# Performance work log

Measured on AMD Instinct MI355X. Metric: run time of the kernel, lower is better.

Reference implementation:

```python
import jax, jax.numpy as jnp
import numpy as np

NUM_CLASSES = 80
STRIDES = (8, 16, 32)


def bce_logits(x, t):
    # numerically stable BCEWithLogits, reduction='none'
    return jnp.maximum(x, 0.) - x * t + jnp.log1p(jnp.exp(-jnp.abs(x)))


def decode_level(feat, stride):
    # feat: [B, C, H, W] -> decoded [B, HW, C], grid x/y [HW], strides [HW]
    B, C, H, W = feat.shape
    out = feat.reshape(B, C, H * W).transpose(0, 2, 1)  # [B, HW, C]
    yv, xv = jnp.meshgrid(jnp.arange(H), jnp.arange(W), indexing='ij')
    grid = jnp.stack([xv, yv], axis=-1).reshape(-1, 2).astype(feat.dtype)  # [HW, 2]
    xy = (out[..., :2] + grid[None]) * stride
    wh = jnp.exp(out[..., 2:4]) * stride
    out = jnp.concatenate([xy, wh, out[..., 4:]], axis=-1)
    return out, grid[:, 0], grid[:, 1], jnp.full((H * W,), float(stride), feat.dtype)


def pairwise_iou_cxcywh(g, p):
    # g: [G,4] gt boxes, p: [A,4] pred boxes (cx,cy,w,h) -> [G,A]
    tl = jnp.maximum(g[:, None, :2] - g[:, None, 2:] * 0.5, p[None, :, :2] - p[None, :, 2:] * 0.5)
    br = jnp.minimum(g[:, None, :2] + g[:, None, 2:] * 0.5, p[None, :, :2] + p[None, :, 2:] * 0.5)
    area_g = g[:, 2] * g[:, 3]
    area_p = p[:, 2] * p[:, 3]
    en = jnp.all(tl < br, axis=-1)
    inter = jnp.prod(br - tl, axis=-1) * en
    return inter / (area_g[:, None] + area_p[None, :] - inter + 1e-16)


def simota_assign(gt_boxes, gt_cls, bbox_p, cls_p, obj_p, xc, yc, strides):
    # per-image SimOTA label assignment (masked, jit-friendly)
    # gt_boxes [G,4], gt_cls [G] int, bbox_p [A,4], cls_p [A,C], obj_p [A,1]
    G = gt_boxes.shape[0]
    A = bbox_p.shape[0]
    gl = gt_boxes[:, 0:1] - 0.5 * gt_boxes[:, 2:3]
    gr = gt_boxes[:, 0:1] + 0.5 * gt_boxes[:, 2:3]
    gt_ = gt_boxes[:, 1:2] - 0.5 * gt_boxes[:, 3:4]
    gb = gt_boxes[:, 1:2] + 0.5 * gt_boxes[:, 3:4]
    in_box = (xc[None] > gl) & (xc[None] < gr) & (yc[None] > gt_) & (yc[None] < gb)  # [G,A]
    r = 2.5 * strides[None]
    in_ctr = ((xc[None] > gt_boxes[:, 0:1] - r) & (xc[None] < gt_boxes[:, 0:1] + r)
              & (yc[None] > gt_boxes[:, 1:2] - r) & (yc[None] < gt_boxes[:, 1:2] + r))
    geom = in_box | in_ctr
    anchor_ok = jnp.any(geom, axis=0)        # fg_mask candidate anchors [A]
    in_both = in_box & in_ctr                # [G,A]

    ious = pairwise_iou_cxcywh(gt_boxes, bbox_p)            # [G,A]
    ious = jnp.where(anchor_ok[None], ious, 0.)
    iou_cost = -jnp.log(ious + 1e-8)

    eps = 1e-8
    p = jnp.sqrt(jax.nn.sigmoid(cls_p) * jax.nn.sigmoid(obj_p))  # [A,C]
    logp = jnp.log(p + eps)
    log1mp = jnp.log(1. - p + eps)
    base = -jnp.sum(log1mp, axis=-1)                              # [A]
    sel = (logp - log1mp)[:, gt_cls]                              # [A,G]
    cls_cost = base[None, :] - sel.T                              # [G,A] = BCE(p, onehot).sum(-1)

    cost = cls_cost + 3.0 * iou_cost + 100000.0 * (~in_both) + 1e9 * (~anchor_ok[None])

    n_cand = min(10, A)
    topk_ious = jax.lax.top_k(ious, n_cand)[0]                    # [G,10]
    dyn_k = jnp.maximum(jnp.sum(topk_ious, axis=1).astype(jnp.int32), 1)  # [G]
    rank = jnp.argsort(jnp.argsort(cost, axis=1), axis=1)         # rank of each anchor per gt
    matching = (rank < dyn_k[:, None]) & anchor_ok[None]          # [G,A] bool

    am = jnp.sum(matching, axis=0)                                # anchors matched to >1 gt
    argmin_g = jnp.argmin(cost, axis=0)                           # [A]
    best = jnp.arange(G)[:, None] == argmin_g[None]               # [G,A]
    matching = jnp.where(am[None] > 1, best, matching)

    fg = jnp.any(matching, axis=0)                                # [A]
    matched_gt = jnp.argmax(matching, axis=0)                     # [A]
    pred_iou = jnp.sum(matching * ious, axis=0)                   # [A]
    cls_t = jax.nn.one_hot(gt_cls[matched_gt], NUM_CLASSES, dtype=bbox_p.dtype) * pred_iou[:, None]
    reg_t = gt_boxes[matched_gt]                                  # [A,4]
    return fg, cls_t, reg_t


def iou_elem(p, t):
    # elementwise IoU between matched pred/target boxes (cxcywh), IOUloss 'iou'
    tl = jnp.maximum(p[..., :2] - p[..., 2:] * 0.5, t[..., :2] - t[..., 2:] * 0.5)
    br = jnp.minimum(p[..., :2] + p[..., 2:] * 0.5, t[..., :2] + t[..., 2:] * 0.5)
    ap = p[..., 2] * p[..., 3]
    ag = t[..., 2] * t[..., 3]
    en = jnp.all(tl < br, axis=-1).astype(p.dtype)
    ai = jnp.prod(br - tl, axis=-1) * en
    return ai / (ap + ag - ai + 1e-16)


def yolo_loss(feat8, feat16, feat32, labels):
    outs, xs, ys, ss = [], [], [], []
    for feat, s in zip((feat8, feat16, feat32), STRIDES):
        o, x, y, st = decode_level(feat, s)
        outs.append(o); xs.append(x); ys.append(y); ss.append(st)
    outputs = jnp.concatenate(outs, axis=1)            # [B, A, 5+C]
    x_shifts = jnp.concatenate(xs)
    y_shifts = jnp.concatenate(ys)
    strides = jnp.concatenate(ss)
    xc = (x_shifts + 0.5) * strides                    # anchor centers [A]
    yc = (y_shifts + 0.5) * strides

    bbox_preds = outputs[..., :4]
    obj_preds = outputs[..., 4]
    cls_preds = outputs[..., 5:5 + NUM_CLASSES]

    labels_sg = jax.lax.stop_gradient(labels)
    gt_boxes = labels_sg[..., :4]
    gt_cls = labels_sg[..., 4].astype(jnp.int32)

    # assignment is @torch.no_grad in the original -> stop_gradient on its inputs
    fg, cls_t, reg_t = jax.vmap(simota_assign, in_axes=(0, 0, 0, 0, 0, None, None, None))(
        gt_boxes, gt_cls,
        jax.lax.stop_gradient(bbox_preds),
        jax.lax.stop_gradient(cls_preds),
        jax.lax.stop_gradient(outputs[..., 4:5]),
        xc, yc, strides)

    fg_f = fg.astype(outputs.dtype)                    # [B, A]
    iou = iou_elem(bbox_preds, reg_t)                  # [B, A]
    loss_iou = jnp.sum(fg_f * (1. - iou ** 2))
    loss_obj = jnp.sum(bce_logits(obj_preds, fg_f))
    loss_cls = jnp.sum(fg_f[..., None] * bce_logits(cls_preds, cls_t))
    num_fg = jnp.maximum(jnp.sum(fg_f), 1.)
    loss = (5.0 * loss_iou + 0.1 * loss_obj + loss_cls) / num_fg
    return loss


def setup_inputs() -> dict:
    key = jax.random.key(0)
    k1, k2, k3, k4, k5, k6, k7 = jax.random.split(key, 7)
    B, G = 32, 30
    feat8 = jax.random.normal(k1, (B, 85, 80, 80), jnp.float32)
    feat16 = jax.random.normal(k2, (B, 85, 40, 40), jnp.float32)
    feat32 = jax.random.normal(k3, (B, 85, 20, 20), jnp.float32)
    cx = jax.random.uniform(k4, (B, G, 1), jnp.float32, 60., 580.)
    cy = jax.random.uniform(k5, (B, G, 1), jnp.float32, 60., 580.)
    wh = jax.random.uniform(k6, (B, G, 2), jnp.float32, 20., 150.)
    cls = jax.random.randint(k7, (B, G, 1), 0, NUM_CLASSES).astype(jnp.float32)
    labels = jnp.concatenate([cx, cy, wh, cls], axis=-1)   # [B, G, 5] = cx,cy,w,h,cls
    return {"feat8": feat8, "feat16": feat16, "feat32": feat32, "labels": labels}


def reference(feat8, feat16, feat32, labels):
    return yolo_loss(feat8, feat16, feat32, labels)
```

## Files before the change

kernel.cpp:

```cpp
#include <hip/hip_runtime.h>
#include <cstdint>
#include <cstddef>

#define NB 32
#define NG 30
#define NA 8400
#define NC 80
#define SELB 512
#define MGRIDX 33
#define NBLK (MGRIDX * NB)
#define LCAP 128
#define NITER 17

typedef unsigned long long u64;

struct Params {
  const float* f8; const float* f16; const float* f32; const float* lab;
  float*    bbox;
  float*    objlog;
  float*    po;
  float*    base_;
  uint2*    gob;
  unsigned* mmask;
  float*    part;
  float*    out;
};

__device__ __forceinline__ float fsigm(float x) {
  return __fdividef(1.0f, 1.0f + __expf(-x));
}

__device__ __forceinline__ void anchor_geom(int a, int& x, int& y, int& W, int& hw,
                                            float& stride, int& lvl) {
  if (a < 6400)      { W = 80; hw = 6400; stride = 8.f;  lvl = 0; int i = a;        y = i / 80; x = i - y * 80; }
  else if (a < 8000) { W = 40; hw = 1600; stride = 16.f; lvl = 1; int i = a - 6400; y = i / 40; x = i - y * 40; }
  else               { W = 20; hw = 400;  stride = 32.f; lvl = 2; int i = a - 8000; y = i / 20; x = i - y * 20; }
}

__device__ __forceinline__ float pair_iou(float px, float py, float pw, float ph,
                                          float glx, float gty, float grx, float gby,
                                          float area_g) {
  float tlx = fmaxf(glx, px - pw * 0.5f);
  float tly = fmaxf(gty, py - ph * 0.5f);
  float brx = fminf(grx, px + pw * 0.5f);
  float bry = fminf(gby, py + ph * 0.5f);
  float inter = ((tlx < brx) && (tly < bry)) ? (brx - tlx) * (bry - tly) : 0.0f;
  return __fdividef(inter, area_g + pw * ph - inter + 1e-16f);
}

__device__ __forceinline__ float cost_of(float4 pb, float po, float bs, unsigned gb,
                                         int g, float glx, float gty, float grx,
                                         float gby, float area_g, float xl,
                                         float& iou_out) {
  bool ok = (gb >> 31) & 1u;
  float iou = pair_iou(pb.x, pb.y, pb.z, pb.w, glx, gty, grx, gby, area_g);
  iou = ok ? iou : 0.0f;
  float iou_cost = -__logf(iou + 1e-8f);
  float pc = fsigm(xl);
  float pr = sqrtf(pc * po);
  float cls_cost = bs - (__logf(pr + 1e-8f) - __logf(1.0f - pr + 1e-8f));
  float c = cls_cost + 3.0f * iou_cost;
  c = c + (((gb >> g) & 1u) ? 0.0f : 100000.0f);
  c = c + (ok ? 0.0f : 1000000000.0f);
  iou_out = iou;
  return c;
}

__device__ __forceinline__ u64 packkey(float c, int a) {
  unsigned b = __float_as_uint(c);
  b = (b & 0x80000000u) ? ~b : (b | 0x80000000u);
  return ((u64)b << 32) | (unsigned)a;
}

__device__ float base_of(const Params& p, int b, int a, float po) {
  int lvl = (a < 6400) ? 0 : (a < 8000) ? 1 : 2;
  int hw  = (lvl == 0) ? 6400 : (lvl == 1) ? 1600 : 400;
  int loff = (lvl == 0) ? 0 : (lvl == 1) ? 6400 : 8000;
  const float* f = (lvl == 0) ? p.f8 : (lvl == 1) ? p.f16 : p.f32;
  int cb = b * 85 * hw + 5 * hw + (a - loff);
  float bs = 0.0f;
#pragma unroll 1
  for (int c = 0; c < NC; c++) {
    float xl = f[cb + c * hw];
    float pc = fsigm(xl);
    float pr = sqrtf(pc * po);
    bs -= __logf(1.0f - pr + 1e-8f);
  }
  return bs;
}

__global__ __launch_bounds__(256) void k_stage(Params p) {
  __shared__ float sglx[NG], sgrx[NG], sgty[NG], sgby[NG], sgx[NG], sgy[NG];
  int b = blockIdx.y;
  int tid = threadIdx.x;
  if (tid < NG) {
    const float* gt = p.lab + (b * NG + tid) * 5;
    float gx = gt[0], gy = gt[1], gw = gt[2], gh = gt[3];
    sgx[tid] = gx; sgy[tid] = gy;
    sglx[tid] = gx - 0.5f * gw; sgrx[tid] = gx + 0.5f * gw;
    sgty[tid] = gy - 0.5f * gh; sgby[tid] = gy + 0.5f * gh;
  }
  __syncthreads();
  int a = blockIdx.x * 256 + tid;
  if (a >= NA) return;
  p.mmask[b * NA + a] = 0u;

  int x, y, W, hw, lvl; float stride;
  anchor_geom(a, x, y, W, hw, stride, lvl);
  const float* f = (lvl == 0) ? p.f8 : (lvl == 1) ? p.f16 : p.f32;
  int loff = (lvl == 0) ? 0 : (lvl == 1) ? 6400 : 8000;
  int fb = b * 85 * hw + (a - loff);

  float tx = f[fb];
  float ty = f[fb + hw];
  float tw = f[fb + 2 * hw];
  float th = f[fb + 3 * hw];
  float ob = f[fb + 4 * hw];

  float px = (tx + (float)x) * stride;
  float py = (ty + (float)y) * stride;
  float pw = __expf(tw) * stride;
  float ph = __expf(th) * stride;
  ((float4*)p.bbox)[b * NA + a] = make_float4(px, py, pw, ph);
  p.objlog[b * NA + a] = ob;
  float po_r = fsigm(ob);
  p.po[b * NA + a] = po_r;

  float xc = ((float)x + 0.5f) * stride;
  float yc = ((float)y + 0.5f) * stride;
  float r = 2.5f * stride;
  float plx = px - 0.5f * pw, prx = px + 0.5f * pw;
  float pty = py - 0.5f * ph, pby = py + 0.5f * ph;
  unsigned gb = 0, ov = 0; int ok = 0;
#pragma unroll
  for (int g = 0; g < NG; g++) {
    float glx = sglx[g], grx = sgrx[g], gty_ = sgty[g], gby = sgby[g];
    float gx = sgx[g], gy = sgy[g];
    bool inb = (xc > glx) && (xc < grx) && (yc > gty_) && (yc < gby);
    bool inc = (xc > gx - r) && (xc < gx + r) && (yc > gy - r) && (yc < gy + r);
    ok |= (inb || inc) ? 1 : 0;
    gb |= (unsigned)(inb && inc) << g;
    bool o = (fmaxf(glx, plx) < fminf(grx, prx)) && (fmaxf(gty_, pty) < fminf(gby, pby));
    ov |= (unsigned)o << g;
  }
  unsigned gbw = gb | ((unsigned)ok << 31);
  p.gob[b * NA + a] = make_uint2(gbw, ok ? ov : 0u);

  if (gb & 0x3FFFFFFFu) {
    int cb = fb + 5 * hw;
    float bs = 0.0f;
#pragma unroll
    for (int c = 0; c < NC; c++) {
      float xl = f[cb + c * hw];
      float pc = fsigm(xl);
      float pr = sqrtf(pc * po_r);
      bs -= __logf(1.0f - pr + 1e-8f);
    }
    p.base_[b * NA + a] = bs;
  }
}

__device__ __forceinline__ u64 block_min_u64(u64 k, int tid, u64* swk) {
#pragma unroll
  for (int off = 32; off; off >>= 1) {
    u64 k2 = __shfl_down(k, off, 64);
    if (k2 < k) k = k2;
  }
  int wv = tid >> 6;
  if ((tid & 63) == 0) swk[wv] = k;
  __syncthreads();
  u64 m = swk[0];
#pragma unroll
  for (int w = 1; w < SELB / 64; w++) if (swk[w] < m) m = swk[w];
  __syncthreads();
  return m;
}

__global__ __launch_bounds__(SELB) void k_sel(Params p) {
  __shared__ float sh_iou[NA];
  __shared__ unsigned sh_cand[LCAP];
  __shared__ float swv[SELB / 64];
  __shared__ int   swi[SELB / 64];
  __shared__ u64   swk[SELB / 64];
  __shared__ int   sh_excl[10];
  __shared__ int   scnt, scand;
  int bg = blockIdx.x;
  int b = bg / NG, g = bg % NG;
  int tid = threadIdx.x;
  if (tid == 0) { scnt = 0; scand = 0; }

  const float* gt = p.lab + (b * NG + g) * 5;
  float gx = gt[0], gy = gt[1], gw = gt[2], gh = gt[3];
  int cg = (int)gt[4];
  float glx = gx - 0.5f * gw, grx = gx + 0.5f * gw;
  float gty = gy - 0.5f * gh, gby = gy + 0.5f * gh;
  float area_g = gw * gh;
  const float4* bb  = (const float4*)p.bbox + b * NA;
  const uint2*  gov = p.gob + b * NA;
  __syncthreads();

  int lane = tid & 63;
  for (int it = 0; it < NITER; it++) {
    int a = it * SELB + tid;
    unsigned ob = 0u, gbw = 0u;
    if (a < NA) { uint2 v = gov[a]; gbw = v.x; ob = v.y; }
    bool act = (ob >> g) & 1u;
    bool cnd = (gbw >> g) & 1u;
    u64 bal = __ballot(act);
    if (bal) {
      int leader = __ffsll(bal) - 1;
      int basec = 0;
      if (lane == leader) basec = atomicAdd(&scnt, __popcll(bal));
      basec = __shfl(basec, leader, 64);
      if (act) {
        int pre = __popcll(bal & ((1ull << lane) - 1ull));
        float4 pb = bb[a];
        float iou = pair_iou(pb.x, pb.y, pb.z, pb.w, glx, gty, grx, gby, area_g);
        sh_iou[basec + pre] = iou;
      }
    }
    u64 bc = __ballot(cnd);
    if (bc) {
      int leader = __ffsll(bc) - 1;
      int basec = 0;
      if (lane == leader) basec = atomicAdd(&scand, __popcll(bc));
      basec = __shfl(basec, leader, 64);
      if (cnd) {
        int s = basec + __popcll(bc & ((1ull << lane) - 1ull));
        if (s < LCAP) sh_cand[s] = (unsigned)a;
      }
    }
  }
  __syncthreads();
  int n = scnt;

  float sum = 0.0f;
  for (int rnd = 0; rnd < 10; rnd++) {
    float mv = -1.0f; int mi = -1;
    for (int j = tid; j < n; j += SELB) {
      float v = sh_iou[j];
      if (v > mv) { mv = v; mi = j; }
    }
#pragma unroll
    for (int off = 32; off; off >>= 1) {
      float v2 = __shfl_down(mv, off, 64);
      int   i2 = __shfl_down(mi, off, 64);
      if (v2 > mv) { mv = v2; mi = i2; }
    }
    if ((tid & 63) == 0) { swv[tid >> 6] = mv; swi[tid >> 6] = mi; }
    __syncthreads();
    float bv = swv[0]; int bi = swi[0];
#pragma unroll
    for (int w = 1; w < SELB / 64; w++)
      if (swv[w] > bv) { bv = swv[w]; bi = swi[w]; }
    sum += fmaxf(bv, 0.0f);
    if (tid == 0 && bi >= 0) sh_iou[bi] = -1.0f;
    __syncthreads();
  }
  int dynk = (int)sum;
  if (dynk < 1) dynk = 1;

  int nc = scand; if (nc > LCAP) nc = LCAP;
  u64 key = ~0ull;
  if (tid < nc) {
    int a = (int)sh_cand[tid];
    float4 pb = bb[a];
    float po_ = p.po[b * NA + a];
    float bs_ = p.base_[b * NA + a];
    unsigned gb_ = gov[a].x;
    int lvl = (a < 6400) ? 0 : (a < 8000) ? 1 : 2;
    int hw  = (lvl == 0) ? 6400 : (lvl == 1) ? 1600 : 400;
    int loff = (lvl == 0) ? 0 : (lvl == 1) ? 6400 : 8000;
    const float* f = (lvl == 0) ? p.f8 : (lvl == 1) ? p.f16 : p.f32;
    float xl = f[b * 85 * hw + (5 + cg) * hw + (a - loff)];
    float iou_;
    float c = cost_of(pb, po_, bs_, gb_, g, glx, gty, grx, gby, area_g, xl, iou_);
    key = packkey(c, a);
  }
  unsigned* mrow = p.mmask + b * NA;
  unsigned gbit = 1u << g;
  int matched = 0;
  for (int it = 0; it < dynk; it++) {
    u64 win = block_min_u64(key, tid, swk);
    if (win == ~0ull) break;
    if (key == win) {
      atomicOr(&mrow[(unsigned)(win & 0xFFFFFFFFu)], gbit);
      key = ~0ull;
    }
    matched++;
  }

  if (matched < dynk) {
    const float* pov = p.po + b * NA;
    for (int it = matched; it < dynk; it++) {
      u64 best = ~0ull;
      for (int al = tid; al < NA; al += SELB) {
        unsigned gb = gov[al].x;
        if (!(gb >> 31)) continue;
        if ((gb >> g) & 1u) continue;
        bool skip = false;
        for (int e = matched; e < it; e++) if (sh_excl[e] == al) skip = true;
        if (skip) continue;
        float po_ = pov[al];
        float bs = base_of(p, b, al, po_);
        int lvl = (al < 6400) ? 0 : (al < 8000) ? 1 : 2;
        int hw  = (lvl == 0) ? 6400 : (lvl == 1) ? 1600 : 400;
        int loff = (lvl == 0) ? 0 : (lvl == 1) ? 6400 : 8000;
        const float* f = (lvl == 0) ? p.f8 : (lvl == 1) ? p.f16 : p.f32;
        float xl = f[b * 85 * hw + (5 + cg) * hw + (al - loff)];
        float4 pb = bb[al];
        float iou_;
        float c = cost_of(pb, po_, bs, gb, g, glx, gty, grx, gby, area_g, xl, iou_);
        u64 nk = packkey(c, al);
        if (nk < best) best = nk;
      }
      u64 win = block_min_u64(best, tid, swk);
      if (win == ~0ull) break;
      int aw = (int)(win & 0xFFFFFFFFu);
      if (best == win) {
        atomicOr(&mrow[aw], gbit);
        p.base_[b * NA + aw] = base_of(p, b, aw, pov[aw]);
      }
      if (tid == 0) sh_excl[it] = aw;
      __syncthreads();
    }
  }
}

__device__ __forceinline__ float block_sum(float val, volatile float* sw) {
#pragma unroll
  for (int off = 32; off > 0; off >>= 1) val += __shfl_down(val, off, 64);
  int lane = threadIdx.x & 63, wv = threadIdx.x >> 6;
  __syncthreads();
  if (lane == 0) sw[wv] = val;
  __syncthreads();
  float r = 0.0f;
  if (threadIdx.x == 0) r = sw[0] + sw[1] + sw[2] + sw[3];
  return r;
}

__global__ __launch_bounds__(256) void k_match(Params p) {
  __shared__ float sred[4];
  int b = blockIdx.y;
  int tid = threadIdx.x;
  int lane = tid & 63;
  int a = blockIdx.x * 256 + tid;
  bool valid = a < NA;

  float l_iou = 0.0f, l_obj = 0.0f, l_cls = 0.0f, l_nfg = 0.0f;
  unsigned mask = 0; int am = 0;
  bool fg = false; float pred_iou = 0.0f; int cg_ = 0;

  if (valid) {
    mask = p.mmask[b * NA + a];
    am = __popc(mask);
    fg = (mask != 0u);
    float ol = p.objlog[b * NA + a];
    float tfg = fg ? 1.0f : 0.0f;
    l_obj = fmaxf(ol, 0.0f) - ol * tfg + __logf(1.0f + __expf(-fabsf(ol)));
  }

  unsigned long long amb = __ballot(valid && am > 1);
  while (amb) {
    int src = __ffsll(amb) - 1;
    amb &= amb - 1ull;
    int aa = __shfl(a, src, 64);
    float4 pb = ((const float4*)p.bbox)[b * NA + aa];
    float po_ = p.po[b * NA + aa];
    float bs_ = p.base_[b * NA + aa];
    unsigned gb_ = p.gob[b * NA + aa].x;

    int lvl = (aa < 6400) ? 0 : (aa < 8000) ? 1 : 2;
    int hw  = (lvl == 0) ? 6400 : (lvl == 1) ? 1600 : 400;
    int loff = (lvl == 0) ? 0 : (lvl == 1) ? 6400 : 8000;
    const float* f = (lvl == 0) ? p.f8 : (lvl == 1) ? p.f16 : p.f32;
    int cb = b * 85 * hw + 5 * hw + (aa - loff);

    float c = 3.4e38f; int gg = 0x7FFFFFFF;
    if (lane < NG) {
      const float* gtg = p.lab + (b * NG + lane) * 5;
      float gx = gtg[0], gy = gtg[1], gw = gtg[2], gh = gtg[3];
      int cg = (int)gtg[4];
      float xl = f[cb + cg * hw];
      float iou_;
      c = cost_of(pb, po_, bs_, gb_, lane,
                  gx - 0.5f * gw, gy - 0.5f * gh,
                  gx + 0.5f * gw, gy + 0.5f * gh, gw * gh, xl, iou_);
      gg = lane;
    }
#pragma unroll
    for (int off = 32; off; off >>= 1) {
      float c2 = __shfl_down(c, off, 64);
      int   g2 = __shfl_down(gg, off, 64);
      if (c2 < c || (c2 == c && g2 < gg)) { c = c2; gg = g2; }
    }
    gg = __shfl(gg, 0, 64);
    if (lane == src) mask = 1u << gg;
  }

  if (valid && fg) {
    l_nfg = 1.0f;
    int mg = __ffs(mask) - 1;
    const float* gtm = p.lab + (b * NG + mg) * 5;
    float gx = gtm[0], gy = gtm[1], gw = gtm[2], gh = gtm[3];
    cg_ = (int)gtm[4];
    float4 pb = ((const float4*)p.bbox)[b * NA + a];
    float iou = pair_iou(pb.x, pb.y, pb.z, pb.w,
                         gx - 0.5f * gw, gy - 0.5f * gh,
                         gx + 0.5f * gw, gy + 0.5f * gh, gw * gh);
    pred_iou = iou;
    l_iou = 1.0f - iou * iou;
  }

  unsigned long long fgb = __ballot(valid && fg);
  while (fgb) {
    int src = __ffsll(fgb) - 1;
    fgb &= fgb - 1ull;
    int   aa   = __shfl(a, src, 64);
    float piou = __shfl(pred_iou, src, 64);
    int   ccg  = __shfl(cg_, src, 64);

    int lvl = (aa < 6400) ? 0 : (aa < 8000) ? 1 : 2;
    int hw  = (lvl == 0) ? 6400 : (lvl == 1) ? 1600 : 400;
    int loff = (lvl == 0) ? 0 : (lvl == 1) ? 6400 : 8000;
    const float* f = (lvl == 0) ? p.f8 : (lvl == 1) ? p.f16 : p.f32;
    int cb = b * 85 * hw + 5 * hw + (aa - loff);

    float part = 0.0f;
#pragma unroll
    for (int c0 = 0; c0 < NC; c0 += 64) {
      int c = c0 + lane;
      if (c < NC) {
        float xl = f[cb + c * hw];
        float t = (c == ccg) ? piou : 0.0f;
        part += fmaxf(xl, 0.0f) - xl * t + __logf(1.0f + __expf(-fabsf(xl)));
      }
    }
#pragma unroll
    for (int off = 32; off; off >>= 1) part += __shfl_down(part, off, 64);
    if (lane == 0) l_cls += part;
  }

  float s0 = block_sum(l_iou, sred);
  float s1 = block_sum(l_obj, sred);
  float s2 = block_sum(l_cls, sred);
  float s3 = block_sum(l_nfg, sred);
  if (tid == 0) {
    ((float4*)p.part)[b * MGRIDX + blockIdx.x] = make_float4(s0, s1, s2, s3);
  }
}

__global__ __launch_bounds__(256) void k_final(Params p) {
  __shared__ float sred[4];
  int tid = threadIdx.x;
  float s0 = 0.0f, s1 = 0.0f, s2 = 0.0f, s3 = 0.0f;
  for (int i = tid; i < NBLK; i += 256) {
    float4 v = ((const float4*)p.part)[i];
    s0 += v.x; s1 += v.y; s2 += v.z; s3 += v.w;
  }
  s0 = block_sum(s0, sred);
  s1 = block_sum(s1, sred);
  s2 = block_sum(s2, sred);
  s3 = block_sum(s3, sred);
  if (tid == 0) {
    p.out[0] = (5.0f * s0 + 0.1f * s1 + s2) / fmaxf(s3, 1.0f);
  }
}

extern "C" void kernel_launch(void* const* d_in, const int* in_sizes, int n_in,
                              void* d_out, int out_size, void* d_ws, size_t ws_size,
                              hipStream_t stream) {
  Params p;
  p.f8  = (const float*)d_in[0];
  p.f16 = (const float*)d_in[1];
  p.f32 = (const float*)d_in[2];
  p.lab = (const float*)d_in[3];

  float* w = (float*)d_ws;
  p.bbox   = w;              w += (size_t)NB * NA * 4;
  p.objlog = w;              w += (size_t)NB * NA;
  p.po     = w;              w += (size_t)NB * NA;
  p.base_  = w;              w += (size_t)NB * NA;
  p.gob    = (uint2*)w;      w += (size_t)NB * NA * 2;
  p.mmask  = (unsigned*)w;   w += (size_t)NB * NA;
  p.part   = w;              w += (size_t)NBLK * 4;
  p.out    = (float*)d_out;

  dim3 gd(MGRIDX, NB);
  k_stage<<<gd, 256, 0, stream>>>(p);
  k_sel  <<<NB * NG, SELB, 0, stream>>>(p);
  k_match<<<gd, 256, 0, stream>>>(p);
  k_final<<<1, 256, 0, stream>>>(p);
}
```

Before: 183.7 us.

## Redistribute per-anchor class cost loop across wavefront lanes via ballot

The 80-class base cost for anchors inside both box and center regions was computed serially by the owning thread, leaving the rest of the wavefront idle under divergence. Now each wave ballots the qualifying anchors and processes them one at a time, with all 64 lanes loading and transforming different classes, followed by a shuffle-based sum. This should cut divergence for sparse candidates. The cost is a sequential shuffle reduction per anchor, which could be slow when many anchors in a wave qualify. The summation order also changes, so results may differ slightly in float.

```diff
diff --git a/kernel.cpp b/kernel.cpp
--- a/kernel.cpp
+++ b/kernel.cpp
@@ -102,61 +102,81 @@
   }
   __syncthreads();
   int a = blockIdx.x * 256 + tid;
-  if (a >= NA) return;
-  p.mmask[b * NA + a] = 0u;
-
+  bool valid = a < NA;
+  int lane = tid & 63;
+
+  unsigned gb = 0, ov = 0; int ok = 0;
+  float po_r = 0.0f;
   int x, y, W, hw, lvl; float stride;
-  anchor_geom(a, x, y, W, hw, stride, lvl);
+  anchor_geom(valid ? a : NA - 1, x, y, W, hw, stride, lvl);
   const float* f = (lvl == 0) ? p.f8 : (lvl == 1) ? p.f16 : p.f32;
   int loff = (lvl == 0) ? 0 : (lvl == 1) ? 6400 : 8000;
-  int fb = b * 85 * hw + (a - loff);
-
-  float tx = f[fb];
-  float ty = f[fb + hw];
-  float tw = f[fb + 2 * hw];
-  float th = f[fb + 3 * hw];
-  float ob = f[fb + 4 * hw];
-
-  float px = (tx + (float)x) * stride;
-  float py = (ty + (float)y) * stride;
-  float pw = __expf(tw) * stride;
-  float ph = __expf(th) * stride;
-  ((float4*)p.bbox)[b * NA + a] = make_float4(px, py, pw, ph);
-  p.objlog[b * NA + a] = ob;
-  float po_r = fsigm(ob);
-  p.po[b * NA + a] = po_r;
-
-  float xc = ((float)x + 0.5f) * stride;
-  float yc = ((float)y + 0.5f) * stride;
-  float r = 2.5f * stride;
-  float plx = px - 0.5f * pw, prx = px + 0.5f * pw;
-  float pty = py - 0.5f * ph, pby = py + 0.5f * ph;
-  unsigned gb = 0, ov = 0; int ok = 0;
-#pragma unroll
-  for (int g = 0; g < NG; g++) {
-    float glx = sglx[g], grx = sgrx[g], gty_ = sgty[g], gby = sgby[g];
-    float gx = sgx[g], gy = sgy[g];
-    bool inb = (xc > glx) && (xc < grx) && (yc > gty_) && (yc < gby);
-    bool inc = (xc > gx - r) && (xc < gx + r) && (yc > gy - r) && (yc < gy + r);
-    ok |= (inb || inc) ? 1 : 0;
-    gb |= (unsigned)(inb && inc) << g;
-    bool o = (fmaxf(glx, plx) < fminf(grx, prx)) && (fmaxf(gty_, pty) < fminf(gby, pby));
-    ov |= (unsigned)o << g;
-  }
-  unsigned gbw = gb | ((unsigned)ok << 31);
-  p.gob[b * NA + a] = make_uint2(gbw, ok ? ov : 0u);
-
-  if (gb & 0x3FFFFFFFu) {
-    int cb = fb + 5 * hw;
+  int fb = b * 85 * hw + ((valid ? a : NA - 1) - loff);
+
+  if (valid) {
+    p.mmask[b * NA + a] = 0u;
+
+    float tx = f[fb];
+    float ty = f[fb + hw];
+    float tw = f[fb + 2 * hw];
+    float th = f[fb + 3 * hw];
+    float ob = f[fb + 4 * hw];
+
+    float px = (tx + (float)x) * stride;
+    float py = (ty + (float)y) * stride;
+    float pw = __expf(tw) * stride;
+    float ph = __expf(th) * stride;
+    ((float4*)p.bbox)[b * NA + a] = make_float4(px, py, pw, ph);
+    p.objlog[b * NA + a] = ob;
+    po_r = fsigm(ob);
+    p.po[b * NA + a] = po_r;
+
+    float xc = ((float)x + 0.5f) * stride;
+    float yc = ((float)y + 0.5f) * stride;
+    float r = 2.5f * stride;
+    float plx = px - 0.5f * pw, prx = px + 0.5f * pw;
+    float pty = py - 0.5f * ph, pby = py + 0.5f * ph;
+#pragma unroll
+    for (int g = 0; g < NG; g++) {
+      float glx = sglx[g], grx = sgrx[g], gty_ = sgty[g], gby = sgby[g];
+      float gx = sgx[g], gy = sgy[g];
+      bool inb = (xc > glx) && (xc < grx) && (yc > gty_) && (yc < gby);
+      bool inc = (xc > gx - r) && (xc < gx + r) && (yc > gy - r) && (yc < gy + r);
+      ok |= (inb || inc) ? 1 : 0;
+      gb |= (unsigned)(inb && inc) << g;
+      bool o = (fmaxf(glx, plx) < fminf(grx, prx)) && (fmaxf(gty_, pty) < fminf(gby, pby));
+      ov |= (unsigned)o << g;
+    }
+    unsigned gbw = gb | ((unsigned)ok << 31);
+    p.gob[b * NA + a] = make_uint2(gbw, ok ? ov : 0u);
+  }
+
+  bool has = valid && (gb & 0x3FFFFFFFu);
+  u64 bal = __ballot(has);
+  while (bal) {
+    int src = __ffsll(bal) - 1;
+    bal &= bal - 1ull;
+    int aa = __shfl(a, src, 64);
+    float po_s = __shfl(po_r, src, 64);
+    int lvl2 = (aa < 6400) ? 0 : (aa < 8000) ? 1 : 2;
+    int hw2  = (lvl2 == 0) ? 6400 : (lvl2 == 1) ? 1600 : 400;
+    int loff2 = (lvl2 == 0) ? 0 : (lvl2 == 1) ? 6400 : 8000;
+    const float* f2 = (lvl2 == 0) ? p.f8 : (lvl2 == 1) ? p.f16 : p.f32;
+    int cb = b * 85 * hw2 + 5 * hw2 + (aa - loff2);
+
+    float xl0 = f2[cb + lane * hw2];
+    float t0 = __logf(1.0f - sqrtf(fsigm(xl0) * po_s) + 1e-8f);
+    float t1 = 0.0f;
+    if (lane < NC - 64) {
+      float xl1 = f2[cb + (64 + lane) * hw2];
+      t1 = __logf(1.0f - sqrtf(fsigm(xl1) * po_s) + 1e-8f);
+    }
     float bs = 0.0f;
 #pragma unroll
-    for (int c = 0; c < NC; c++) {
-      float xl = f[cb + c * hw];
-      float pc = fsigm(xl);
-      float pr = sqrtf(pc * po_r);
-      bs -= __logf(1.0f - pr + 1e-8f);
-    }
-    p.base_[b * NA + a] = bs;
+    for (int c = 0; c < 64; c++) bs -= __shfl(t0, c, 64);
+#pragma unroll
+    for (int c = 0; c < NC - 64; c++) bs -= __shfl(t1, c, 64);
+    if (lane == src) p.base_[b * NA + aa] = bs;
   }
 }
 
```

After: 219.2 us. 1.19x slower.
